# Optimization experiments

Hardware: AMD Instinct MI355X
Metric: run time of the kernel (lower is better)

## Reference

```python
import jax, jax.numpy as jnp
import numpy as np

N, E, G, F_IN = 50000, 200000, 2000, 373
NEG_SLOPE, BN_EPS = 0.2, 1e-5


def _bn(x, g, b, m, v):
    # BatchNorm1d in eval mode with running stats
    return (x - m) * jax.lax.rsqrt(v + BN_EPS) * g + b


def _gcn(x, src, dst, w, b):
    # PyG GCNConv: add self loops, sym-normalize D^-1/2 (A+I) D^-1/2, then aggregate.
    n = x.shape[0]
    h = x @ w  # [N, out]
    deg = jax.ops.segment_sum(jnp.ones_like(src, jnp.float32), dst, n) + 1.0  # +1 self loop
    dinv = jax.lax.rsqrt(deg)
    agg = jax.ops.segment_sum((dinv[src] * dinv[dst])[:, None] * h[src], dst, n)
    # self-loop contribution has norm dinv[i]^2
    return agg + (dinv * dinv)[:, None] * h + b


def _gat(x, src, dst, w, a_s, a_d, b, H, C):
    # PyG GATConv (concat=True): per-edge attention logits, segment softmax over
    # incoming edges (incl. self loop, handled analytically), scatter-add aggregate.
    n = x.shape[0]
    h = (x @ w).reshape(n, H, C)  # [N, H, C]
    al_s = jnp.einsum('nhc,hc->nh', h, a_s)  # source-side logit term
    al_d = jnp.einsum('nhc,hc->nh', h, a_d)  # dest-side logit term
    e = jax.nn.leaky_relu(al_s[src] + al_d[dst], NEG_SLOPE)  # [E, H]
    e_self = jax.nn.leaky_relu(al_s + al_d, NEG_SLOPE)       # [N, H] self-loop logit
    m = jnp.maximum(jax.ops.segment_max(e, dst, n), e_self)  # stable softmax max
    we = jnp.exp(e - m[dst])
    ws = jnp.exp(e_self - m)
    denom = jax.ops.segment_sum(we, dst, n) + ws
    out = jax.ops.segment_sum(we[:, :, None] * h[src], dst, n) + ws[:, :, None] * h
    return (out / denom[:, :, None]).reshape(n, H * C) + b


def _forward(fl, edge_index, batch):
    (x, gw1, gb1, gw2, gb2, gw3, gb3,
     g01g, g01b, g01m, g01v, g02g, g02b, g02m, g02v, g03g, g03b, g03m, g03v,
     aw1, as1, ad1, ab1, aw2, as2, ad2, ab2, aw3, as3, ad3, ab3,
     g11g, g11b, g11m, g11v, g12g, g12b, g12m, g12v, g13g, g13b, g13m, g13v,
     f1w, f1b, f2w, f2b, f3w, f3b) = fl
    src, dst = edge_index[0], edge_index[1]
    xg = _bn(jax.nn.relu(_gcn(x, src, dst, gw1, gb1)), g01g, g01b, g01m, g01v)
    xg = _bn(jax.nn.relu(_gcn(xg, src, dst, gw2, gb2)), g02g, g02b, g02m, g02v)
    xg = _bn(jax.nn.relu(_gcn(xg, src, dst, gw3, gb3)), g03g, g03b, g03m, g03v)
    xg = jax.ops.segment_sum(xg, batch, G)  # global_add_pool -> [G, 128]
    y = _bn(jax.nn.relu(_gat(x, src, dst, aw1, as1, ad1, ab1, 3, 256)), g11g, g11b, g11m, g11v)
    y = _bn(jax.nn.relu(_gat(y, src, dst, aw2, as2, ad2, ab2, 3, 128)), g12g, g12b, g12m, g12v)
    y = _bn(jax.nn.relu(_gat(y, src, dst, aw3, as3, ad3, ab3, 3, 128)), g13g, g13b, g13m, g13v)
    y = jax.ops.segment_sum(y, batch, G)  # [G, 384]
    cr = jnp.concatenate([xg, y], axis=1)  # [G, 512]
    cr = jax.nn.relu(cr @ f1w + f1b)  # dropout is identity in eval mode
    cr = jax.nn.relu(cr @ f2w + f2b)
    cr = jax.nn.relu(cr @ f3w + f3b)
    return cr.reshape(-1)  # [G]


def setup_inputs() -> dict:
    key = jax.random.key(0)
    keys = jax.random.split(key, 80)
    ki = iter(range(80))
    def nrm(shape, s=0.05):
        return jax.random.normal(keys[next(ki)], shape, jnp.float32) * s
    inp = {}
    inp['x'] = jax.random.normal(keys[next(ki)], (N, F_IN), jnp.float32)
    inp['edge_index'] = jax.random.randint(keys[next(ki)], (2, E), 0, N, dtype=jnp.int32)
    inp['batch'] = jnp.sort(jax.random.randint(keys[next(ki)], (N,), 0, G, dtype=jnp.int32))
    for i, o, t in [(373, 256, '1'), (256, 128, '2'), (128, 128, '3')]:
        inp['gw' + t] = nrm((i, o))
        inp['gb' + t] = jnp.zeros((o,), jnp.float32)
    for t, d in [('01', 256), ('02', 128), ('03', 128), ('11', 768), ('12', 384), ('13', 384)]:
        inp['g' + t + 'g'] = jnp.ones((d,), jnp.float32)
        inp['g' + t + 'b'] = jnp.zeros((d,), jnp.float32)
        inp['g' + t + 'm'] = nrm((d,))
        inp['g' + t + 'v'] = jax.random.uniform(keys[next(ki)], (d,), jnp.float32) + 0.5
    for i, o, t in [(373, 256, '1'), (768, 128, '2'), (384, 128, '3')]:
        inp['aw' + t] = nrm((i, 3 * o))
        inp['as' + t] = nrm((3, o))
        inp['ad' + t] = nrm((3, o))
        inp['ab' + t] = jnp.zeros((3 * o,), jnp.float32)
    for i, o, t in [(512, 256, '1'), (256, 64, '2'), (64, 1, '3')]:
        inp['f' + t + 'w'] = nrm((i, o))
        inp['f' + t + 'b'] = jnp.zeros((o,), jnp.float32)
    return inp


def reference(x, gw1, gb1, gw2, gb2, gw3, gb3,
              g01g, g01b, g01m, g01v, g02g, g02b, g02m, g02v, g03g, g03b, g03m, g03v,
              aw1, as1, ad1, ab1, aw2, as2, ad2, ab2, aw3, as3, ad3, ab3,
              g11g, g11b, g11m, g11v, g12g, g12b, g12m, g12v, g13g, g13b, g13m, g13v,
              f1w, f1b, f2w, f2b, f3w, f3b, edge_index, batch):
    fl = (x, gw1, gb1, gw2, gb2, gw3, gb3,
          g01g, g01b, g01m, g01v, g02g, g02b, g02m, g02v, g03g, g03b, g03m, g03v,
          aw1, as1, ad1, ab1, aw2, as2, ad2, ab2, aw3, as3, ad3, ab3,
          g11g, g11b, g11m, g11v, g12g, g12b, g12m, g12v, g13g, g13b, g13m, g13v,
          f1w, f1b, f2w, f2b, f3w, f3b)
    return _forward(fl, edge_index, batch)
```

## Files before the change

### kernel.cpp

```cpp
#include <hip/hip_runtime.h>
#include <cstdint>
#include <cstddef>

#define N_NODES 50000
#define N_EDGES 200000
#define N_GRAPHS 2000
#define F_IN 373
#define NEG_SLOPE 0.2f
#define BN_EPS 1e-5f

typedef float f32x4 __attribute__((ext_vector_type(4)));
typedef float f32x2 __attribute__((ext_vector_type(2)));
typedef short s16x8 __attribute__((ext_vector_type(8)));
typedef short s16x4 __attribute__((ext_vector_type(4)));
typedef unsigned int u32x4 __attribute__((ext_vector_type(4)));
typedef unsigned int u32x2 __attribute__((ext_vector_type(2)));

template <int VPT> struct VecT;
template <> struct VecT<2> { using type = f32x2; };
template <> struct VecT<4> { using type = f32x4; };
template <int VPT> struct UVecT;
template <> struct UVecT<2> { using type = u32x2; };
template <> struct UVecT<4> { using type = u32x4; };

static inline int cdiv(long long a, long long b) { return (int)((a + b - 1) / b); }

__device__ __forceinline__ float lrelu(float x) { return x > 0.f ? x : NEG_SLOPE * x; }

__device__ __forceinline__ void atomAddF(float* p, float v) {
#if defined(__HIP_DEVICE_COMPILE__)
  unsafeAtomicAdd(p, v);
#else
  atomicAdd(p, v);
#endif
}

__device__ __forceinline__ unsigned short bf16rne(float f) {
  unsigned u = __float_as_uint(f);
  unsigned r = u + 0x7fffu + ((u >> 16) & 1u);
  return (unsigned short)(r >> 16);
}
__device__ __forceinline__ void split2(float f, unsigned short& hi, unsigned short& lo) {
  hi = bf16rne(f);
  float fh = __uint_as_float(((unsigned)hi) << 16);
  lo = bf16rne(f - fh);
}
__device__ __forceinline__ unsigned packsplit(float f) {
  unsigned short hi, lo;
  split2(f, hi, lo);
  return (((unsigned)hi) << 16) | (unsigned)lo;
}
__device__ __forceinline__ float unpackf(unsigned w) {
  return __uint_as_float(w & 0xffff0000u) + __uint_as_float(w << 16);
}

#define SEGSZ 136
__device__ __forceinline__ int ebase(int row, int k) {
  return ((row >> 4) * 4 + (k >> 3)) * SEGSZ + ((row & 15) << 3) + (k & 7);
}

__global__ void k_zero(float* p, long long n) {
  long long i = (long long)blockIdx.x * blockDim.x + threadIdx.x;
  if (i < n) p[i] = 0.f;
}
__global__ void k_zero_i(int* p, int n) {
  int i = blockIdx.x * blockDim.x + threadIdx.x;
  if (i < n) p[i] = 0;
}
__global__ void k_deg(int* __restrict__ deg, const int* __restrict__ dst, int e) {
  int i = blockIdx.x * blockDim.x + threadIdx.x;
  if (i < e) atomicAdd(&deg[dst[i]], 1);
}
__global__ void k_dinv(const int* __restrict__ deg, float* __restrict__ dinv, int n) {
  int i = blockIdx.x * blockDim.x + threadIdx.x;
  if (i < n) dinv[i] = rsqrtf((float)deg[i] + 1.0f);
}

__global__ void k_scan(const int* __restrict__ deg, int* __restrict__ rowptr,
                       int* __restrict__ cursor, int n) {
  __shared__ int wsum[16];
  __shared__ int carry_s;
  const int lane = threadIdx.x & 63;
  const int wid = threadIdx.x >> 6;
  if (threadIdx.x == 0) carry_s = 0;
  __syncthreads();
  for (int base = 0; base < n; base += 1024) {
    int i = base + threadIdx.x;
    int v = (i < n) ? deg[i] : 0;
    int s = v;
#pragma unroll
    for (int off = 1; off < 64; off <<= 1) {
      int t = __shfl_up(s, off);
      if (lane >= off) s += t;
    }
    if (lane == 63) wsum[wid] = s;
    __syncthreads();
    if (threadIdx.x == 0) {
      int acc = carry_s;
#pragma unroll
      for (int w = 0; w < 16; w++) { int t = wsum[w]; wsum[w] = acc; acc += t; }
      carry_s = acc;
    }
    __syncthreads();
    if (i < n) { rowptr[i] = wsum[wid] + s - v; cursor[i] = 0; }
    __syncthreads();
  }
  if (threadIdx.x == 0) rowptr[n] = carry_s;
}

__global__ void k_csr_scatter(const int* __restrict__ src, const int* __restrict__ dst,
                              const int* __restrict__ rowptr, int* __restrict__ cursor,
                              int* __restrict__ csr_src, int e) {
  int i = blockIdx.x * blockDim.x + threadIdx.x;
  if (i >= e) return;
  int d = dst[i];
  int pos = rowptr[d] + atomicAdd(&cursor[d], 1);
  csr_src[pos] = src[i];
}

__global__ void k_buildwt(const float* __restrict__ W, int ldW, int col0, int Nsub,
                          int K, int Kpad, unsigned* __restrict__ Wt) {
  int n = blockIdx.x * blockDim.x + threadIdx.x;
  int k = blockIdx.y;
  if (n >= Nsub) return;
  float v = (k < K) ? W[(size_t)k * ldW + col0 + n] : 0.f;
  Wt[(size_t)n * Kpad + k] = packsplit(v);
}

__global__ __launch_bounds__(256) void k_mfma_gemm(
    const float* __restrict__ Ap, int lda, int amode, int Kact,
    const unsigned* __restrict__ Wt, int Kpad,
    float* __restrict__ C, int M, int ldC, int col0,
    const float* __restrict__ a_s, const float* __restrict__ a_d,
    float* __restrict__ als, float* __restrict__ ald, int lshift) {
  __shared__ unsigned short Ah[16 * SEGSZ], Al[16 * SEGSZ];
  __shared__ unsigned short Bh[32 * SEGSZ], Bl[32 * SEGSZ];
  const int bm = blockIdx.y * 64;
  const int bn = blockIdx.x * 128;
  const int tid = threadIdx.x;
  const int lane = tid & 63;
  const int wave = tid >> 6;
  const int wm = wave & 1;
  const int wn = wave >> 1;

  f32x4 acc[2][4];
#pragma unroll
  for (int i = 0; i < 2; i++)
#pragma unroll
    for (int j = 0; j < 4; j++) acc[i][j] = (f32x4){0.f, 0.f, 0.f, 0.f};

  const int srow = tid >> 3;
  const int skq = (tid & 7) << 2;

  for (int k0 = 0; k0 < Kpad; k0 += 32) {
#pragma unroll
    for (int i = 0; i < 2; i++) {
      int row = i * 32 + srow;
      int grow = bm + row;
      unsigned short hv[4], lv[4];
      if (amode == 1) {
        u32x4 v = (grow < M) ? *(const u32x4*)((const unsigned*)Ap + (size_t)grow * lda + k0 + skq)
                             : (u32x4){0u, 0u, 0u, 0u};
#pragma unroll
        for (int u = 0; u < 4; u++) { hv[u] = (unsigned short)(v[u] >> 16); lv[u] = (unsigned short)(v[u] & 0xffffu); }
      } else if (amode == 2) {
        f32x4 v = (grow < M) ? *(const f32x4*)(Ap + (size_t)grow * lda + k0 + skq)
                             : (f32x4){0.f, 0.f, 0.f, 0.f};
#pragma unroll
        for (int u = 0; u < 4; u++) split2(v[u], hv[u], lv[u]);
      } else {
        const float* ap = Ap + (size_t)grow * lda;
#pragma unroll
        for (int u = 0; u < 4; u++) {
          int kc = k0 + skq + u;
          float f = (grow < M && kc < Kact) ? ap[kc] : 0.f;
          split2(f, hv[u], lv[u]);
        }
      }
      int eb = ebase(row, skq);
      *(s16x4*)&Ah[eb] = *(s16x4*)hv;
      *(s16x4*)&Al[eb] = *(s16x4*)lv;
    }
#pragma unroll
    for (int i = 0; i < 4; i++) {
      int row = i * 32 + srow;
      u32x4 v = *(const u32x4*)(Wt + (size_t)(bn + row) * Kpad + k0 + skq);
      unsigned short hv[4], lv[4];
#pragma unroll
      for (int u = 0; u < 4; u++) { hv[u] = (unsigned short)(v[u] >> 16); lv[u] = (unsigned short)(v[u] & 0xffffu); }
      int eb = ebase(row, skq);
      *(s16x4*)&Bh[eb] = *(s16x4*)hv;
      *(s16x4*)&Bl[eb] = *(s16x4*)lv;
    }
    __syncthreads();
    const int koct = lane >> 4;
    const int mrow = lane & 15;
    s16x8 ah[2], al[2];
#pragma unroll
    for (int g = 0; g < 2; g++) {
      int ab = ((wm * 2 + g) * 4 + koct) * SEGSZ + (mrow << 3);
      ah[g] = *(const s16x8*)&Ah[ab];
      al[g] = *(const s16x8*)&Al[ab];
    }
#pragma unroll
    for (int j = 0; j < 4; j++) {
      int bb = ((wn * 4 + j) * 4 + koct) * SEGSZ + (mrow << 3);
      s16x8 bhj = *(const s16x8*)&Bh[bb];
      s16x8 blj = *(const s16x8*)&Bl[bb];
#pragma unroll
      for (int g = 0; g < 2; g++) {
        acc[g][j] = __builtin_amdgcn_mfma_f32_16x16x32_bf16(ah[g], bhj, acc[g][j], 0, 0, 0);
        acc[g][j] = __builtin_amdgcn_mfma_f32_16x16x32_bf16(al[g], bhj, acc[g][j], 0, 0, 0);
        acc[g][j] = __builtin_amdgcn_mfma_f32_16x16x32_bf16(ah[g], blj, acc[g][j], 0, 0, 0);
      }
    }
    __syncthreads();
  }
  const int mrow = lane & 15;
  const int rq = (lane >> 4) << 2;
  float asv[4], adv[4];
  if (a_s) {
#pragma unroll
    for (int j = 0; j < 4; j++) {
      int c = bn + wn * 64 + j * 16 + mrow;
      asv[j] = a_s[c];
      adv[j] = a_d[c];
    }
  }
  const int head = bn >> lshift;
#pragma unroll
  for (int g = 0; g < 2; g++) {
#pragma unroll
    for (int r = 0; r < 4; r++) {
      int row = bm + wm * 32 + g * 16 + rq + r;
      bool rok = row < M;
      float ps = 0.f, pd = 0.f;
#pragma unroll
      for (int j = 0; j < 4; j++) {
        int ccol = bn + wn * 64 + j * 16 + mrow;
        float v = acc[g][j][r];
        if (rok) C[(size_t)row * ldC + col0 + ccol] = v;
        ps += v * asv[j];
        pd += v * adv[j];
      }
      if (a_s) {
#pragma unroll
        for (int off = 1; off < 16; off <<= 1) {
          ps += __shfl_xor(ps, off);
          pd += __shfl_xor(pd, off);
        }
        if (mrow == 0 && rok) {
          atomAddF(&als[(size_t)head * N_NODES + row], ps);
          atomAddF(&ald[(size_t)head * N_NODES + row], pd);
        }
      }
    }
  }
}

__global__ __launch_bounds__(256) void k_gemm(
    const float* __restrict__ A, const float* __restrict__ W,
    const float* __restrict__ bias, float* __restrict__ C,
    int M, int K, int Nsub, int ldW, int ldC, int col0, int flags) {
  __shared__ float As[16][68];
  __shared__ float Bs[16][68];
  const int bm = blockIdx.y * 64;
  const int bn = blockIdx.x * 64;
  const int tid = threadIdx.x;
  const int tm = (tid >> 4) << 2;
  const int tn = (tid & 15) << 2;
  float acc[4][4] = {};
  for (int k0 = 0; k0 < K; k0 += 16) {
    {
      int idx = tid * 4;
      int row = idx >> 4;
      int kk = idx & 15;
      const float* ap = A + (size_t)(bm + row) * K + k0 + kk;
      bool rok = (bm + row) < M;
#pragma unroll
      for (int i = 0; i < 4; i++) {
        int kcur = k0 + kk + i;
        As[kk + i][row] = (rok && kcur < K) ? ap[i] : 0.f;
      }
    }
#pragma unroll
    for (int i = 0; i < 4; i++) {
      int idx = tid + i * 256;
      int kk = idx >> 6;
      int nn = idx & 63;
      int kcur = k0 + kk;
      Bs[kk][nn] = (kcur < K && (bn + nn) < Nsub)
                       ? W[(size_t)kcur * ldW + col0 + bn + nn] : 0.f;
    }
    __syncthreads();
#pragma unroll
    for (int kk = 0; kk < 16; kk++) {
      float av[4], bv[4];
#pragma unroll
      for (int i = 0; i < 4; i++) av[i] = As[kk][tm + i];
#pragma unroll
      for (int j = 0; j < 4; j++) bv[j] = Bs[kk][tn + j];
#pragma unroll
      for (int i = 0; i < 4; i++)
#pragma unroll
        for (int j = 0; j < 4; j++) acc[i][j] += av[i] * bv[j];
    }
    __syncthreads();
  }
#pragma unroll
  for (int i = 0; i < 4; i++) {
    int row = bm + tm + i;
    if (row >= M) continue;
#pragma unroll
    for (int j = 0; j < 4; j++) {
      int col = bn + tn + j;
      if (col >= Nsub) continue;
      float v = acc[i][j];
      if (flags & 1) v += bias[col0 + col];
      if (flags & 2) v = fmaxf(v, 0.f);
      C[(size_t)row * ldC + col] = v;
    }
  }
}

template <int VPT>
__global__ __launch_bounds__(256) void k_gcn_fused(
    const float* __restrict__ h, const float* __restrict__ dinv,
    const int* __restrict__ rowptr, const int* __restrict__ csr_src,
    const float* __restrict__ bias, const float* __restrict__ g,
    const float* __restrict__ b, const float* __restrict__ m,
    const float* __restrict__ vv, unsigned* __restrict__ out, int n, int F) {
  using V = typename VecT<VPT>::type;
  using UV = typename UVecT<VPT>::type;
  int wid = (blockIdx.x * blockDim.x + threadIdx.x) >> 6;
  int lane = threadIdx.x & 63;
  if (wid >= n) return;
  const int fo = lane * VPT;
  float dd = dinv[wid];
  V acc = *(const V*)(h + (size_t)wid * F + fo) * (dd * dd) + *(const V*)(bias + fo);
  int e0 = rowptr[wid], e1 = rowptr[wid + 1];
  for (int e = e0; e < e1; e++) {
    int s = csr_src[e];
    float w = dinv[s] * dd;
    acc += *(const V*)(h + (size_t)s * F + fo) * w;
  }
  V mg = *(const V*)(m + fo);
  V vg = *(const V*)(vv + fo);
  V gg = *(const V*)(g + fo);
  V bg = *(const V*)(b + fo);
  UV res;
#pragma unroll
  for (int u = 0; u < VPT; u++) {
    float val = fmaxf(acc[u], 0.f);
    res[u] = packsplit((val - mg[u]) * rsqrtf(vg[u] + BN_EPS) * gg[u] + bg[u]);
  }
  *(UV*)(out + (size_t)wid * F + fo) = res;
}

template <int VPT>
__global__ __launch_bounds__(256) void k_gat_fused(
    const float* __restrict__ h, int ldH,
    const float* __restrict__ als, const float* __restrict__ ald,
    const int* __restrict__ rowptr, const int* __restrict__ csr_src,
    const float* __restrict__ bias, const float* __restrict__ g,
    const float* __restrict__ b, const float* __restrict__ m,
    const float* __restrict__ vv, unsigned* __restrict__ out, int ldO, int col0, int n) {
  using V = typename VecT<VPT>::type;
  using UV = typename UVecT<VPT>::type;
  int wid = (blockIdx.x * blockDim.x + threadIdx.x) >> 6;
  int lane = threadIdx.x & 63;
  if (wid >= n) return;
  const int co = lane * VPT;
  float aldd = ald[wid];
  float self_lg = lrelu(als[wid] + aldd);
  int e0 = rowptr[wid], e1 = rowptr[wid + 1];
  float mx = self_lg;
  for (int e = e0; e < e1; e++) {
    mx = fmaxf(mx, lrelu(als[csr_src[e]] + aldd));
  }
  float den = __expf(self_lg - mx);
  V acc = *(const V*)(h + (size_t)wid * ldH + co) * den;
  for (int e = e0; e < e1; e++) {
    int s = csr_src[e];
    float w = __expf(lrelu(als[s] + aldd) - mx);
    den += w;
    acc += *(const V*)(h + (size_t)s * ldH + co) * w;
  }
  float rden = 1.f / den;
  const int fo = col0 + co;
  V bi = *(const V*)(bias + fo);
  V mg = *(const V*)(m + fo);
  V vg = *(const V*)(vv + fo);
  V gg = *(const V*)(g + fo);
  V bg = *(const V*)(b + fo);
  UV res;
#pragma unroll
  for (int u = 0; u < VPT; u++) {
    float val = fmaxf(acc[u] * rden + bi[u], 0.f);
    res[u] = packsplit((val - mg[u]) * rsqrtf(vg[u] + BN_EPS) * gg[u] + bg[u]);
  }
  *(UV*)(out + (size_t)wid * ldO + fo) = res;
}

__global__ void k_pool_add(float* __restrict__ pooled, const unsigned* __restrict__ act,
                           const int* __restrict__ batch, int n, int F, int off) {
  long long idx = (long long)blockIdx.x * blockDim.x + threadIdx.x;
  if (idx >= (long long)n * F) return;
  int node = (int)(idx / F);
  int f = (int)(idx % F);
  atomAddF(&pooled[(size_t)batch[node] * 512 + off + f], unpackf(act[idx]));
}
__global__ void k_fc3(const float* __restrict__ in, const float* __restrict__ w,
                      const float* __restrict__ b, float* __restrict__ out, int g) {
  int wid = (blockIdx.x * blockDim.x + threadIdx.x) >> 6;
  int lane = threadIdx.x & 63;
  if (wid >= g) return;
  float v = in[wid * 64 + lane] * w[lane];
#pragma unroll
  for (int off = 32; off > 0; off >>= 1) v += __shfl_down(v, off);
  if (lane == 0) out[wid] = fmaxf(v + b[0], 0.f);
}

static void gemm_fp32(hipStream_t s, const float* A, const float* W, const float* bias,
                      float* C, int M, int K, int Nsub, int ldW, int ldC, int col0, int flags) {
  dim3 grid(cdiv(Nsub, 64), cdiv(M, 64));
  k_gemm<<<grid, 256, 0, s>>>(A, W, bias, C, M, K, Nsub, ldW, ldC, col0, flags);
}

static void gemm_mfma(hipStream_t s, const void* A, int lda, int amode,
                      const float* W, int ldW, int wcol0, int K, int Kpad,
                      unsigned* Wt, float* C, int M, int Nsub, int ldC, int ccol0,
                      const float* a_s = nullptr, const float* a_d = nullptr,
                      float* als = nullptr, float* ald = nullptr, int lshift = 30) {
  dim3 wg(cdiv(Nsub, 256), Kpad);
  k_buildwt<<<wg, 256, 0, s>>>(W, ldW, wcol0, Nsub, K, Kpad, Wt);
  dim3 grid(Nsub / 128, cdiv(M, 64));
  k_mfma_gemm<<<grid, 256, 0, s>>>((const float*)A, lda, amode, K, Wt, Kpad, C, M, ldC, ccol0,
                                   a_s, a_d, als, ald, lshift);
}

extern "C" void kernel_launch(void* const* d_in, const int* in_sizes, int n_in,
                              void* d_out, int out_size, void* d_ws, size_t ws_size,
                              hipStream_t stream) {
  const float* x = (const float*)d_in[0];
  const int* ei = (const int*)d_in[1];
  const int* batch = (const int*)d_in[2];
  const float* gw1 = (const float*)d_in[3];  const float* gb1 = (const float*)d_in[4];
  const float* gw2 = (const float*)d_in[5];  const float* gb2 = (const float*)d_in[6];
  const float* gw3 = (const float*)d_in[7];  const float* gb3 = (const float*)d_in[8];
  const float* g01g = (const float*)d_in[9];  const float* g01b = (const float*)d_in[10];
  const float* g01m = (const float*)d_in[11]; const float* g01v = (const float*)d_in[12];
  const float* g02g = (const float*)d_in[13]; const float* g02b = (const float*)d_in[14];
  const float* g02m = (const float*)d_in[15]; const float* g02v = (const float*)d_in[16];
  const float* g03g = (const float*)d_in[17]; const float* g03b = (const float*)d_in[18];
  const float* g03m = (const float*)d_in[19]; const float* g03v = (const float*)d_in[20];
  const float* g11g = (const float*)d_in[21]; const float* g11b = (const float*)d_in[22];
  const float* g11m = (const float*)d_in[23]; const float* g11v = (const float*)d_in[24];
  const float* g12g = (const float*)d_in[25]; const float* g12b = (const float*)d_in[26];
  const float* g12m = (const float*)d_in[27]; const float* g12v = (const float*)d_in[28];
  const float* g13g = (const float*)d_in[29]; const float* g13b = (const float*)d_in[30];
  const float* g13m = (const float*)d_in[31]; const float* g13v = (const float*)d_in[32];
  const float* aw1 = (const float*)d_in[33]; const float* as1 = (const float*)d_in[34];
  const float* ad1 = (const float*)d_in[35]; const float* ab1 = (const float*)d_in[36];
  const float* aw2 = (const float*)d_in[37]; const float* as2 = (const float*)d_in[38];
  const float* ad2 = (const float*)d_in[39]; const float* ab2 = (const float*)d_in[40];
  const float* aw3 = (const float*)d_in[41]; const float* as3 = (const float*)d_in[42];
  const float* ad3 = (const float*)d_in[43]; const float* ab3 = (const float*)d_in[44];
  const float* f1w = (const float*)d_in[45]; const float* f1b = (const float*)d_in[46];
  const float* f2w = (const float*)d_in[47]; const float* f2b = (const float*)d_in[48];
  const float* f3w = (const float*)d_in[49]; const float* f3b = (const float*)d_in[50];

  const int* src = ei;
  const int* dst = ei + N_EDGES;

  size_t need = 0;
  need += (size_t)N_NODES * 768;
  need += (size_t)N_NODES * 384;
  need += (size_t)N_NODES;
  need += (size_t)N_NODES * 6;
  need += (size_t)N_NODES + 1;
  need += (size_t)N_EDGES;
  need += (size_t)N_GRAPHS * (512 + 256 + 64);
  if (ws_size < need * sizeof(float)) return;

  float* wp = (float*)d_ws;
  unsigned* OUTP = (unsigned*)wp; wp += (size_t)N_NODES * 768;
  float* H = wp;       wp += (size_t)N_NODES * 384;
  float* dinv = wp;    wp += N_NODES;
  float* als3 = wp;    wp += (size_t)N_NODES * 3;
  float* ald3 = wp;    wp += (size_t)N_NODES * 3;
  int* rowptr = (int*)wp;  wp += N_NODES + 1;
  int* csr_src = (int*)wp; wp += N_EDGES;
  float* pooled = wp; wp += (size_t)N_GRAPHS * 512;
  float* fc1 = wp;    wp += (size_t)N_GRAPHS * 256;
  float* fc2 = wp;    wp += (size_t)N_GRAPHS * 64;
  int* degi = (int*)als3;
  int* cursor = (int*)ald3;
  unsigned* Wt = (unsigned*)fc1;

  k_zero_i<<<cdiv(N_NODES, 256), 256, 0, stream>>>(degi, N_NODES);
  k_deg<<<cdiv(N_EDGES, 256), 256, 0, stream>>>(degi, dst, N_EDGES);
  k_dinv<<<cdiv(N_NODES, 256), 256, 0, stream>>>(degi, dinv, N_NODES);
  k_scan<<<1, 1024, 0, stream>>>(degi, rowptr, cursor, N_NODES);
  k_csr_scatter<<<cdiv(N_EDGES, 256), 256, 0, stream>>>(src, dst, rowptr, cursor, csr_src, N_EDGES);
  k_zero<<<cdiv((long long)N_GRAPHS * 512, 256), 256, 0, stream>>>(pooled, (long long)N_GRAPHS * 512);

  const int nodeWaveGrid = cdiv((long long)N_NODES * 64, 256);

  struct { const float *w, *bias, *g, *b, *m, *v; int F; } gcn[3] = {
    {gw1, gb1, g01g, g01b, g01m, g01v, 256},
    {gw2, gb2, g02g, g02b, g02m, g02v, 128},
    {gw3, gb3, g03g, g03b, g03m, g03v, 128}};
  int gF = F_IN;
  for (int l = 0; l < 3; l++) {
    int F = gcn[l].F;
    if (l == 0)
      gemm_mfma(stream, x, F_IN, 0, gcn[l].w, F, 0, F_IN, 384, Wt, H, N_NODES, F, F, 0);
    else
      gemm_mfma(stream, OUTP, gF, 1, gcn[l].w, F, 0, gF, gF, Wt, H, N_NODES, F, F, 0);
    if (F == 256)
      k_gcn_fused<4><<<nodeWaveGrid, 256, 0, stream>>>(H, dinv, rowptr, csr_src,
          gcn[l].bias, gcn[l].g, gcn[l].b, gcn[l].m, gcn[l].v, OUTP, N_NODES, F);
    else
      k_gcn_fused<2><<<nodeWaveGrid, 256, 0, stream>>>(H, dinv, rowptr, csr_src,
          gcn[l].bias, gcn[l].g, gcn[l].b, gcn[l].m, gcn[l].v, OUTP, N_NODES, F);
    gF = F;
  }
  k_pool_add<<<cdiv((long long)N_NODES * 128, 256), 256, 0, stream>>>(pooled, OUTP, batch, N_NODES, 128, 0);

  {
    int C = 256, HC = 768;
    for (int hh = 0; hh < 3; hh++) {
      k_zero<<<cdiv((long long)N_NODES * 6, 256), 256, 0, stream>>>(als3, (long long)N_NODES * 6);
      gemm_mfma(stream, x, F_IN, 0, aw1, HC, hh * C, F_IN, 384, Wt, H, N_NODES, C, C, 0,
                as1 + hh * C, ad1 + hh * C, als3, ald3, 30);
      k_gat_fused<4><<<nodeWaveGrid, 256, 0, stream>>>(H, C, als3, ald3, rowptr, csr_src,
          ab1, g11g, g11b, g11m, g11v, OUTP, HC, hh * C, N_NODES);
    }
  }

  struct { const float *w, *s, *d, *bias, *g, *b, *m, *v; int K; } gat[2] = {
    {aw2, as2, ad2, ab2, g12g, g12b, g12m, g12v, 768},
    {aw3, as3, ad3, ab3, g13g, g13b, g13m, g13v, 384}};
  for (int l = 0; l < 2; l++) {
    int C = 128, HC = 384;
    k_zero<<<cdiv((long long)N_NODES * 6, 256), 256, 0, stream>>>(als3, (long long)N_NODES * 6);
    gemm_mfma(stream, OUTP, gat[l].K, 1, gat[l].w, HC, 0, gat[l].K, gat[l].K, Wt, H, N_NODES, HC, HC, 0,
              gat[l].s, gat[l].d, als3, ald3, 7);
    for (int hh = 0; hh < 3; hh++) {
      k_gat_fused<2><<<nodeWaveGrid, 256, 0, stream>>>(H + hh * C, HC,
          als3 + (size_t)hh * N_NODES, ald3 + (size_t)hh * N_NODES, rowptr, csr_src,
          gat[l].bias, gat[l].g, gat[l].b, gat[l].m, gat[l].v, OUTP, HC, hh * C, N_NODES);
    }
  }
  k_pool_add<<<cdiv((long long)N_NODES * 384, 256), 256, 0, stream>>>(pooled, OUTP, batch, N_NODES, 384, 128);

  gemm_fp32(stream, pooled, f1w, f1b, fc1, N_GRAPHS, 512, 256, 256, 256, 0, 3);
  gemm_fp32(stream, fc1, f2w, f2b, fc2, N_GRAPHS, 256, 64, 64, 64, 0, 3);
  k_fc3<<<cdiv((long long)N_GRAPHS * 64, 256), 256, 0, stream>>>(fc2, f3w, f3b, (float*)d_out, N_GRAPHS);
}
```

Baseline: 1.748 ms.

## Enlarge MFMA GEMM tile, unroll edge loops, fuse three GAT heads per node

The split-bf16 MFMA GEMM tile grows from 64x128 to 128x128 per block, and the LDS layout drops its padded segment in favour of a dense power-of-two one. This raises the ratio of MFMA work to staging work but doubles accumulator registers and may cause LDS bank conflicts. The GCN and GAT aggregation loops are unrolled by two with separate accumulators to expose more memory-level parallelism. For GAT layers 2 and 3, a new kernel handles all three heads per node in one launch, so each neighbour's index and row pointer are read once instead of three times.

```diff
diff --git a/kernel.cpp b/kernel.cpp
--- a/kernel.cpp
+++ b/kernel.cpp
@@ -54,9 +54,8 @@
   return __uint_as_float(w & 0xffff0000u) + __uint_as_float(w << 16);
 }
 
-#define SEGSZ 136
 __device__ __forceinline__ int ebase(int row, int k) {
-  return ((row >> 4) * 4 + (k >> 3)) * SEGSZ + ((row & 15) << 3) + (k & 7);
+  return ((row >> 4) << 9) + ((k >> 3) << 7) + ((row & 15) << 3) + (k & 7);
 }
 
 __global__ void k_zero(float* p, long long n) {
@@ -133,19 +132,17 @@
     float* __restrict__ C, int M, int ldC, int col0,
     const float* __restrict__ a_s, const float* __restrict__ a_d,
     float* __restrict__ als, float* __restrict__ ald, int lshift) {
-  __shared__ unsigned short Ah[16 * SEGSZ], Al[16 * SEGSZ];
-  __shared__ unsigned short Bh[32 * SEGSZ], Bl[32 * SEGSZ];
-  const int bm = blockIdx.y * 64;
+  __shared__ unsigned short Ah[128 * 32], Al[128 * 32], Bh[128 * 32], Bl[128 * 32];
+  const int bm = blockIdx.y * 128;
   const int bn = blockIdx.x * 128;
   const int tid = threadIdx.x;
   const int lane = tid & 63;
   const int wave = tid >> 6;
-  const int wm = wave & 1;
-  const int wn = wave >> 1;
-
-  f32x4 acc[2][4];
-#pragma unroll
-  for (int i = 0; i < 2; i++)
+  const int wm = wave >> 1, wn = wave & 1;
+
+  f32x4 acc[4][4];
+#pragma unroll
+  for (int i = 0; i < 4; i++)
 #pragma unroll
     for (int j = 0; j < 4; j++) acc[i][j] = (f32x4){0.f, 0.f, 0.f, 0.f};
 
@@ -154,7 +151,7 @@
 
   for (int k0 = 0; k0 < Kpad; k0 += 32) {
 #pragma unroll
-    for (int i = 0; i < 2; i++) {
+    for (int i = 0; i < 4; i++) {
       int row = i * 32 + srow;
       int grow = bm + row;
       unsigned short hv[4], lv[4];
@@ -193,22 +190,21 @@
       *(s16x4*)&Bl[eb] = *(s16x4*)lv;
     }
     __syncthreads();
-    const int koct = lane >> 4;
-    const int mrow = lane & 15;
-    s16x8 ah[2], al[2];
-#pragma unroll
-    for (int g = 0; g < 2; g++) {
-      int ab = ((wm * 2 + g) * 4 + koct) * SEGSZ + (mrow << 3);
+    const int fo = ((lane >> 4) << 7) + ((lane & 15) << 3);
+    s16x8 ah[4], al[4];
+#pragma unroll
+    for (int g = 0; g < 4; g++) {
+      int ab = ((wm * 4 + g) << 9) + fo;
       ah[g] = *(const s16x8*)&Ah[ab];
       al[g] = *(const s16x8*)&Al[ab];
     }
 #pragma unroll
     for (int j = 0; j < 4; j++) {
-      int bb = ((wn * 4 + j) * 4 + koct) * SEGSZ + (mrow << 3);
+      int bb = ((wn * 4 + j) << 9) + fo;
       s16x8 bhj = *(const s16x8*)&Bh[bb];
       s16x8 blj = *(const s16x8*)&Bl[bb];
 #pragma unroll
-      for (int g = 0; g < 2; g++) {
+      for (int g = 0; g < 4; g++) {
         acc[g][j] = __builtin_amdgcn_mfma_f32_16x16x32_bf16(ah[g], bhj, acc[g][j], 0, 0, 0);
         acc[g][j] = __builtin_amdgcn_mfma_f32_16x16x32_bf16(al[g], bhj, acc[g][j], 0, 0, 0);
         acc[g][j] = __builtin_amdgcn_mfma_f32_16x16x32_bf16(ah[g], blj, acc[g][j], 0, 0, 0);
@@ -229,10 +225,10 @@
   }
   const int head = bn >> lshift;
 #pragma unroll
-  for (int g = 0; g < 2; g++) {
+  for (int g = 0; g < 4; g++) {
 #pragma unroll
     for (int r = 0; r < 4; r++) {
-      int row = bm + wm * 32 + g * 16 + rq + r;
+      int row = bm + wm * 64 + g * 16 + rq + r;
       bool rok = row < M;
       float ps = 0.f, pd = 0.f;
 #pragma unroll
@@ -337,13 +333,21 @@
   if (wid >= n) return;
   const int fo = lane * VPT;
   float dd = dinv[wid];
-  V acc = *(const V*)(h + (size_t)wid * F + fo) * (dd * dd) + *(const V*)(bias + fo);
+  V acc0 = *(const V*)(h + (size_t)wid * F + fo) * (dd * dd) + *(const V*)(bias + fo);
+  V acc1 = {};
   int e0 = rowptr[wid], e1 = rowptr[wid + 1];
-  for (int e = e0; e < e1; e++) {
-    int s = csr_src[e];
-    float w = dinv[s] * dd;
-    acc += *(const V*)(h + (size_t)s * F + fo) * w;
-  }
+  int e = e0;
+  for (; e + 1 < e1; e += 2) {
+    int s0 = csr_src[e], s1 = csr_src[e + 1];
+    float w0 = dinv[s0] * dd, w1 = dinv[s1] * dd;
+    acc0 += *(const V*)(h + (size_t)s0 * F + fo) * w0;
+    acc1 += *(const V*)(h + (size_t)s1 * F + fo) * w1;
+  }
+  if (e < e1) {
+    int s0 = csr_src[e];
+    acc0 += *(const V*)(h + (size_t)s0 * F + fo) * (dinv[s0] * dd);
+  }
+  acc0 += acc1;
   V mg = *(const V*)(m + fo);
   V vg = *(const V*)(vv + fo);
   V gg = *(const V*)(g + fo);
@@ -351,7 +355,7 @@
   UV res;
 #pragma unroll
   for (int u = 0; u < VPT; u++) {
-    float val = fmaxf(acc[u], 0.f);
+    float val = fmaxf(acc0[u], 0.f);
     res[u] = packsplit((val - mg[u]) * rsqrtf(vg[u] + BN_EPS) * gg[u] + bg[u]);
   }
   *(UV*)(out + (size_t)wid * F + fo) = res;
@@ -375,17 +379,28 @@
   float self_lg = lrelu(als[wid] + aldd);
   int e0 = rowptr[wid], e1 = rowptr[wid + 1];
   float mx = self_lg;
-  for (int e = e0; e < e1; e++) {
-    mx = fmaxf(mx, lrelu(als[csr_src[e]] + aldd));
-  }
+  for (int e = e0; e < e1; e++) mx = fmaxf(mx, lrelu(als[csr_src[e]] + aldd));
   float den = __expf(self_lg - mx);
-  V acc = *(const V*)(h + (size_t)wid * ldH + co) * den;
-  for (int e = e0; e < e1; e++) {
-    int s = csr_src[e];
-    float w = __expf(lrelu(als[s] + aldd) - mx);
-    den += w;
-    acc += *(const V*)(h + (size_t)s * ldH + co) * w;
-  }
+  V acc0 = *(const V*)(h + (size_t)wid * ldH + co) * den;
+  V acc1 = {};
+  float den1 = 0.f;
+  int e = e0;
+  for (; e + 1 < e1; e += 2) {
+    int s0 = csr_src[e], s1 = csr_src[e + 1];
+    float w0 = __expf(lrelu(als[s0] + aldd) - mx);
+    float w1 = __expf(lrelu(als[s1] + aldd) - mx);
+    den += w0; den1 += w1;
+    acc0 += *(const V*)(h + (size_t)s0 * ldH + co) * w0;
+    acc1 += *(const V*)(h + (size_t)s1 * ldH + co) * w1;
+  }
+  if (e < e1) {
+    int s0 = csr_src[e];
+    float w0 = __expf(lrelu(als[s0] + aldd) - mx);
+    den += w0;
+    acc0 += *(const V*)(h + (size_t)s0 * ldH + co) * w0;
+  }
+  acc0 += acc1;
+  den += den1;
   float rden = 1.f / den;
   const int fo = col0 + co;
   V bi = *(const V*)(bias + fo);
@@ -396,10 +411,65 @@
   UV res;
 #pragma unroll
   for (int u = 0; u < VPT; u++) {
-    float val = fmaxf(acc[u] * rden + bi[u], 0.f);
+    float val = fmaxf(acc0[u] * rden + bi[u], 0.f);
     res[u] = packsplit((val - mg[u]) * rsqrtf(vg[u] + BN_EPS) * gg[u] + bg[u]);
   }
   *(UV*)(out + (size_t)wid * ldO + fo) = res;
+}
+
+__global__ __launch_bounds__(256) void k_gat_fused3(
+    const float* __restrict__ h,
+    const float* __restrict__ als3, const float* __restrict__ ald3,
+    const int* __restrict__ rowptr, const int* __restrict__ csr_src,
+    const float* __restrict__ bias, const float* __restrict__ g,
+    const float* __restrict__ b, const float* __restrict__ m,
+    const float* __restrict__ vv, unsigned* __restrict__ out, int n) {
+  int wid = (blockIdx.x * blockDim.x + threadIdx.x) >> 6;
+  int lane = threadIdx.x & 63;
+  if (wid >= n) return;
+  const int co = lane * 2;
+  float aldd[3], mx[3], den[3];
+  f32x2 acc[3];
+#pragma unroll
+  for (int hh = 0; hh < 3; hh++) {
+    aldd[hh] = ald3[(size_t)hh * N_NODES + wid];
+    mx[hh] = lrelu(als3[(size_t)hh * N_NODES + wid] + aldd[hh]);
+  }
+  int e0 = rowptr[wid], e1 = rowptr[wid + 1];
+  for (int e = e0; e < e1; e++) {
+    int s = csr_src[e];
+#pragma unroll
+    for (int hh = 0; hh < 3; hh++)
+      mx[hh] = fmaxf(mx[hh], lrelu(als3[(size_t)hh * N_NODES + s] + aldd[hh]));
+  }
+#pragma unroll
+  for (int hh = 0; hh < 3; hh++) {
+    float ws = __expf(lrelu(als3[(size_t)hh * N_NODES + wid] + aldd[hh]) - mx[hh]);
+    den[hh] = ws;
+    acc[hh] = *(const f32x2*)(h + (size_t)wid * 384 + hh * 128 + co) * ws;
+  }
+  for (int e = e0; e < e1; e++) {
+    int s = csr_src[e];
+    const float* hs = h + (size_t)s * 384 + co;
+#pragma unroll
+    for (int hh = 0; hh < 3; hh++) {
+      float w = __expf(lrelu(als3[(size_t)hh * N_NODES + s] + aldd[hh]) - mx[hh]);
+      den[hh] += w;
+      acc[hh] += *(const f32x2*)(hs + hh * 128) * w;
+    }
+  }
+#pragma unroll
+  for (int hh = 0; hh < 3; hh++) {
+    float rden = 1.f / den[hh];
+    int fo = hh * 128 + co;
+    u32x2 res;
+#pragma unroll
+    for (int u = 0; u < 2; u++) {
+      float val = fmaxf(acc[hh][u] * rden + bias[fo + u], 0.f);
+      res[u] = packsplit((val - m[fo + u]) * rsqrtf(vv[fo + u] + BN_EPS) * g[fo + u] + b[fo + u]);
+    }
+    *(u32x2*)(out + (size_t)wid * 384 + fo) = res;
+  }
 }
 
 __global__ void k_pool_add(float* __restrict__ pooled, const unsigned* __restrict__ act,
@@ -434,7 +504,7 @@
                       float* als = nullptr, float* ald = nullptr, int lshift = 30) {
   dim3 wg(cdiv(Nsub, 256), Kpad);
   k_buildwt<<<wg, 256, 0, s>>>(W, ldW, wcol0, Nsub, K, Kpad, Wt);
-  dim3 grid(Nsub / 128, cdiv(M, 64));
+  dim3 grid(Nsub / 128, cdiv(M, 128));
   k_mfma_gemm<<<grid, 256, 0, s>>>((const float*)A, lda, amode, K, Wt, Kpad, C, M, ldC, ccol0,
                                    a_s, a_d, als, ald, lshift);
 }
@@ -543,15 +613,11 @@
     {aw2, as2, ad2, ab2, g12g, g12b, g12m, g12v, 768},
     {aw3, as3, ad3, ab3, g13g, g13b, g13m, g13v, 384}};
   for (int l = 0; l < 2; l++) {
-    int C = 128, HC = 384;
     k_zero<<<cdiv((long long)N_NODES * 6, 256), 256, 0, stream>>>(als3, (long long)N_NODES * 6);
-    gemm_mfma(stream, OUTP, gat[l].K, 1, gat[l].w, HC, 0, gat[l].K, gat[l].K, Wt, H, N_NODES, HC, HC, 0,
+    gemm_mfma(stream, OUTP, gat[l].K, 1, gat[l].w, 384, 0, gat[l].K, gat[l].K, Wt, H, N_NODES, 384, 384, 0,
               gat[l].s, gat[l].d, als3, ald3, 7);
-    for (int hh = 0; hh < 3; hh++) {
-      k_gat_fused<2><<<nodeWaveGrid, 256, 0, stream>>>(H + hh * C, HC,
-          als3 + (size_t)hh * N_NODES, ald3 + (size_t)hh * N_NODES, rowptr, csr_src,
-          gat[l].bias, gat[l].g, gat[l].b, gat[l].m, gat[l].v, OUTP, HC, hh * C, N_NODES);
-    }
+    k_gat_fused3<<<nodeWaveGrid, 256, 0, stream>>>(H, als3, ald3, rowptr, csr_src,
+        gat[l].bias, gat[l].g, gat[l].b, gat[l].m, gat[l].v, OUTP, N_NODES);
   }
   k_pool_add<<<cdiv((long long)N_NODES * 384, 256), 256, 0, stream>>>(pooled, OUTP, batch, N_NODES, 384, 128);
 
```

Result: faster. 1.709 ms (-2.3%).
